# Optimization experiments

Hardware: AMD Instinct MI355X
Metric: run time of the kernel (lower is better)

The kernel has to match this reference:

```python
import jax, jax.numpy as jnp
import numpy as np

N, MA, F, NF = 512, 64, 128, 16
UPDATE_RATIO = 0.1
DECAY = 1.0
EPS = 1e-12  # avoids NaN grad of sqrt at self-distance 0 (torch diagonal is masked out by exp anyway)


def setup_inputs() -> dict:
    key = jax.random.key(0)
    ks = jax.random.split(key, 8)
    z = jax.random.randint(ks[0], (N, MA), 0, 10, dtype=jnp.int64) if jax.config.jax_enable_x64 else jax.random.randint(ks[0], (N, MA), 0, 10, dtype=jnp.int32)
    # pad last few atoms of each molecule with -1 to exercise the mask
    z = z.at[:, MA - 8:].set(-1)
    r = jax.random.normal(ks[1], (N, MA, 3), dtype=jnp.float32) * 3.0
    h = jax.random.normal(ks[2], (N, MA, F), dtype=jnp.float32)
    distances = jnp.linspace(0.5, 6.0, NF, dtype=jnp.float32)
    widths = jax.random.uniform(ks[3], (NF,), dtype=jnp.float32) * 0.5 + 0.5  # keep sigma > 0
    din = F * (1 + NF)  # 2176
    W1 = jax.random.normal(ks[4], (din, 512), dtype=jnp.float32) * (1.0 / np.sqrt(din))
    b1 = jnp.zeros((512,), dtype=jnp.float32)
    W2 = jax.random.normal(ks[5], (512, F), dtype=jnp.float32) * (1.0 / np.sqrt(512.0))
    b2 = jnp.zeros((F,), dtype=jnp.float32)
    return {"z": z, "r": r, "h": h, "distances": distances, "widths": widths,
            "W1": W1, "b1": b1, "W2": W2, "b2": b2}


def reference(z, r, h, distances, widths, W1, b1, W2, b2):
    n, ma = z.shape
    nf = distances.shape[0]
    # pairwise distance: (n, ma, ma)
    dv = r[:, :, None, :] - r[:, None, :, :]
    d = jnp.sqrt(jnp.sum(dv * dv, axis=-1) + EPS)
    mu = distances.reshape(1, nf, 1, 1)
    sigma = widths.reshape(1, nf, 1, 1)
    mask1 = (z > -1).astype(h.dtype)                      # (n, ma)
    pair_mask = mask1[:, :, None] * mask1[:, None, :]     # (n, ma, ma)
    # Gaussian RBF scores, masked: (n, nf, ma, ma)
    w = pair_mask[:, None] * jnp.exp(-((d[:, None] - mu) ** 2) / sigma) * 5.0
    # aggregate neighbor features: (n, ma, nf, F) -> (n, ma, nf*F)
    u = jnp.einsum('nfab,nbc->nafc', w, h).reshape(n, ma, nf * h.shape[-1])
    v = jnp.concatenate([h, u], axis=2)                   # (n, ma, F*(1+nf))
    v = jax.nn.silu(v @ W1 + b1) @ W2 + b2                # MLP 'net'
    h_new = h + v * UPDATE_RATIO * DECAY * mask1[:, :, None]
    return (z, r, h_new)
```

## Files before the change

kernel.cpp:

```cpp
#include <hip/hip_runtime.h>

#define MA 64
#define F 128
#define NF 16
#define HID 512
#define LDUB 144
#define WLB  9216
#define LDWB 144
#define LDT1B 1040

typedef float  float4v __attribute__((ext_vector_type(4)));
typedef short  short8  __attribute__((ext_vector_type(8)));
typedef int    int8v   __attribute__((ext_vector_type(8)));

static __device__ __forceinline__ unsigned int pack2bf(float x, float y) {
    unsigned int a = __float_as_uint(x) + 0x8000u;
    unsigned int b = __float_as_uint(y) + 0x8000u;
    return __builtin_amdgcn_perm(b, a, 0x07060302u);
}
static __device__ __forceinline__ unsigned short f2bf1(float x) {
    return (unsigned short)((__float_as_uint(x) + 0x8000u) >> 16);
}
static __device__ __forceinline__ unsigned int pk4fp8(float a, float b, float c, float d) {
    int p = __builtin_amdgcn_cvt_pk_fp8_f32(a, b, 0, false);
    p = __builtin_amdgcn_cvt_pk_fp8_f32(c, d, p, true);
    return (unsigned int)p;
}

__global__ void pack_frags(const float* __restrict__ W1, const float* __restrict__ W2,
                           unsigned char* __restrict__ w1p, unsigned short* __restrict__ w2p) {
    int gid  = blockIdx.x * 4 + (threadIdx.x >> 6);
    int lane = threadIdx.x & 63;
    int arow = lane & 15;
    int kq   = lane >> 4;
    if (gid < 544) {
        int kt = gid >> 5, jt = gid & 31;
        const float* base = W1 + (size_t)(kt * 128 + kq * 32) * HID + jt * 16 + arow;
        unsigned int o[8];
        #pragma unroll
        for (int p = 0; p < 8; p++)
            o[p] = pk4fp8(base[(p * 4 + 0) * HID], base[(p * 4 + 1) * HID],
                          base[(p * 4 + 2) * HID], base[(p * 4 + 3) * HID]);
        unsigned char* dst = w1p + ((size_t)gid * 64 + lane) * 32;
        *(uint4*)dst        = (uint4){o[0], o[1], o[2], o[3]};
        *(uint4*)(dst + 16) = (uint4){o[4], o[5], o[6], o[7]};
    } else if (gid < 544 + 128) {
        int g2 = gid - 544;
        int kt = g2 >> 3, mt = g2 & 7;
        const float* base = W2 + (size_t)(kt * 32 + kq * 8) * F + mt * 16 + arow;
        short8 o;
        #pragma unroll
        for (int j = 0; j < 8; j++) o[j] = (short)f2bf1(base[j * F]);
        *(short8*)(w2p + ((size_t)g2 * 64 + lane) * 8) = o;
    }
}

__launch_bounds__(512, 2)
__global__ void node_conv_mfma(const int* __restrict__ z, const float* __restrict__ rr,
        const float* __restrict__ h, const float* __restrict__ dist,
        const float* __restrict__ wid, const float* __restrict__ b1,
        const float* __restrict__ b2,
        const unsigned char* __restrict__ w1p, const unsigned short* __restrict__ w2p,
        float* __restrict__ out) {
    const int n = blockIdx.x;
    const int tid = threadIdx.x;
    const int lane = tid & 63;
    const int wave = tid >> 6;
    const int arow = lane & 15;
    const int quad = lane >> 4;
    const int kgrp = quad * 8;

    __shared__ __attribute__((aligned(16))) unsigned char lds[33280];
    __shared__ float r_lds[MA][4];

    const int N = gridDim.x;
    const float* hg = h + (size_t)n * MA * F;

    if (tid < MA) {
        int zi = z[n * MA + tid];
        out[(size_t)n * MA + tid] = (float)zi;
        r_lds[tid][0] = rr[(n * MA + tid) * 3 + 0];
        r_lds[tid][1] = rr[(n * MA + tid) * 3 + 1];
        r_lds[tid][2] = rr[(n * MA + tid) * 3 + 2];
        r_lds[tid][3] = (zi > -1) ? 1.0f : 0.0f;
    }
    if (tid < MA * 3)
        out[(size_t)N * MA + (size_t)n * MA * 3 + tid] = rr[(size_t)n * MA * 3 + tid];

    for (int i = tid; i < MA * F / 4; i += 512) {
        float4 v = ((const float4*)hg)[i];
        int a = i >> 5, c4 = (i & 31) * 4;
        *(unsigned int*)&lds[a * LDUB + c4] = pk4fp8(v.x, v.y, v.z, v.w);
    }
    short8 ah[2];
    {
        int c = wave * 16 + arow;
        #pragma unroll
        for (int ks2 = 0; ks2 < 2; ks2++)
            #pragma unroll
            for (int j = 0; j < 8; j++)
                ah[ks2][j] = (short)f2bf1(hg[(size_t)(ks2 * 32 + kgrp + j) * F + c]);
    }
    __syncthreads();

    const int wa = tid >> 3;
    const int wb0 = (tid & 7) * 8;
    float dpre[8];
    {
        float ax = r_lds[wa][0], ay = r_lds[wa][1], az = r_lds[wa][2];
        float am = r_lds[wa][3];
        #pragma unroll
        for (int j = 0; j < 8; j++) {
            float dx = ax - r_lds[wb0 + j][0];
            float dy = ay - r_lds[wb0 + j][1];
            float dz = az - r_lds[wb0 + j][2];
            float d = sqrtf(dx * dx + dy * dy + dz * dz + 1e-12f);
            float mm = am * r_lds[wb0 + j][3];
            dpre[j] = d + (1.0f - mm) * 1e4f;
        }
    }

    {
        float mu = dist[0];
        float isg = 1.0f / wid[0];
        float e[8];
        #pragma unroll
        for (int j = 0; j < 8; j++) {
            float t = dpre[j] - mu;
            e[j] = 5.0f * __expf(-t * t * isg);
        }
        uint4 wp = { pack2bf(e[0], e[1]), pack2bf(e[2], e[3]),
                     pack2bf(e[4], e[5]), pack2bf(e[6], e[7]) };
        *(uint4*)&lds[WLB + wa * LDWB + wb0 * 2] = wp;
    }
    int8v afr[4];
    #pragma unroll
    for (int mt = 0; mt < 4; mt++)
        afr[mt] = *(const int8v*)(w1p + ((size_t)((wave * 4 + mt) * 64 + lane)) * 32);
    __syncthreads();

    const float4v zf = {0.f, 0.f, 0.f, 0.f};
    float4v acc[4][4];
    #pragma unroll
    for (int i = 0; i < 4; i++)
        #pragma unroll
        for (int jv = 0; jv < 4; jv++) acc[i][jv] = zf;

    for (int f = 0; f <= NF; f++) {
        #pragma unroll
        for (int at = 0; at < 4; at++) {
            int8v bfr = *(const int8v*)&lds[(at * 16 + arow) * LDUB + quad * 32];
            #pragma unroll
            for (int mt = 0; mt < 4; mt++)
                acc[mt][at] = __builtin_amdgcn_mfma_scale_f32_16x16x128_f8f6f4(
                    afr[mt], bfr, acc[mt][at], 0, 0, 0, 127, 0, 127);
        }

        unsigned int udp[4];
        if (f < NF) {
            const unsigned char* pN = w1p + ((size_t)(((f + 1) * 32 + wave * 4) * 64 + lane)) * 32;
            #pragma unroll
            for (int mt = 0; mt < 4; mt++) afr[mt] = *(const int8v*)(pN + mt * 2048);

            float4v ud[4];
            #pragma unroll
            for (int at = 0; at < 4; at++) ud[at] = zf;
            #pragma unroll
            for (int ks2 = 0; ks2 < 2; ks2++)
                #pragma unroll
                for (int at = 0; at < 4; at++) {
                    short8 bw = *(const short8*)&lds[WLB + (at * 16 + arow) * LDWB + (ks2 * 32 + kgrp) * 2];
                    ud[at] = __builtin_amdgcn_mfma_f32_16x16x32_bf16(ah[ks2], bw, ud[at], 0, 0, 0);
                }
            #pragma unroll
            for (int at = 0; at < 4; at++)
                udp[at] = pk4fp8(ud[at][0], ud[at][1], ud[at][2], ud[at][3]);
        }
        __syncthreads();

        if (f < NF) {
            #pragma unroll
            for (int at = 0; at < 4; at++)
                *(unsigned int*)&lds[(at * 16 + arow) * LDUB + wave * 16 + quad * 4] = udp[at];

            if (f <= NF - 2) {
                float mu = dist[f + 1];
                float isg = 1.0f / wid[f + 1];
                float e[8];
                #pragma unroll
                for (int j = 0; j < 8; j++) {
                    float t = dpre[j] - mu;
                    e[j] = 5.0f * __expf(-t * t * isg);
                }
                uint4 wp = { pack2bf(e[0], e[1]), pack2bf(e[2], e[3]),
                             pack2bf(e[4], e[5]), pack2bf(e[6], e[7]) };
                *(uint4*)&lds[WLB + wa * LDWB + wb0 * 2] = wp;
            }
            __syncthreads();
        }
    }

    float4 b1v[4];
    #pragma unroll
    for (int mt = 0; mt < 4; mt++)
        b1v[mt] = *(const float4*)&b1[wave * 64 + mt * 16 + quad * 4];
    float* outh = out + (size_t)N * MA * 4 + (size_t)n * MA * F;

    #pragma unroll
    for (int hh = 0; hh < 2; hh++) {
        if (hh) __syncthreads();
        #pragma unroll
        for (int mt = 0; mt < 4; mt++) {
            #pragma unroll
            for (int ai = 0; ai < 2; ai++) {
                const int at = hh * 2 + ai;
                float xs[4];
                #pragma unroll
                for (int r = 0; r < 4; r++) {
                    float x = acc[mt][at][r] + ((const float*)&b1v[mt])[r];
                    xs[r] = x / (1.0f + __expf(-x));
                }
                uint2 pv = { pack2bf(xs[0], xs[1]), pack2bf(xs[2], xs[3]) };
                *(uint2*)&lds[(ai * 16 + arow) * LDT1B + (wave * 64 + mt * 16 + quad * 4) * 2] = pv;
            }
        }
        __syncthreads();

        float4v g2[2] = {zf, zf};
        for (int ks = 0; ks < 16; ks++) {
            short8 aw2 = *(const short8*)(w2p + ((size_t)(ks * 8 + wave) * 64 + lane) * 8);
            #pragma unroll
            for (int n2 = 0; n2 < 2; n2++) {
                short8 bt = *(const short8*)&lds[(n2 * 16 + arow) * LDT1B + (ks * 32 + kgrp) * 2];
                g2[n2] = __builtin_amdgcn_mfma_f32_16x16x32_bf16(aw2, bt, g2[n2], 0, 0, 0);
            }
        }
        #pragma unroll
        for (int n2 = 0; n2 < 2; n2++) {
            int a = hh * 32 + n2 * 16 + arow;
            int c0 = wave * 16 + quad * 4;
            float m = r_lds[a][3] * 0.1f;
            float4 hv = *(const float4*)&hg[a * F + c0];
            float4 b2v = *(const float4*)&b2[c0];
            float4 res;
            res.x = hv.x + (g2[n2][0] + b2v.x) * m;
            res.y = hv.y + (g2[n2][1] + b2v.y) * m;
            res.z = hv.z + (g2[n2][2] + b2v.z) * m;
            res.w = hv.w + (g2[n2][3] + b2v.w) * m;
            *(float4*)&outh[(size_t)a * F + c0] = res;
        }
    }
}

extern "C" void kernel_launch(void* const* d_in, const int* in_sizes, int n_in,
                              void* d_out, int out_size, void* d_ws, size_t ws_size,
                              hipStream_t stream) {
    const int*   z    = (const int*)d_in[0];
    const float* rr   = (const float*)d_in[1];
    const float* h    = (const float*)d_in[2];
    const float* dist = (const float*)d_in[3];
    const float* wid  = (const float*)d_in[4];
    const float* W1   = (const float*)d_in[5];
    const float* b1   = (const float*)d_in[6];
    const float* W2   = (const float*)d_in[7];
    const float* b2   = (const float*)d_in[8];
    float* out = (float*)d_out;

    int Nmol = in_sizes[0] / MA;

    unsigned char*  w1p = (unsigned char*)d_ws;
    unsigned short* w2p = (unsigned short*)(w1p + (size_t)544 * 64 * 32);

    pack_frags<<<168, 256, 0, stream>>>(W1, W2, w1p, w2p);
    node_conv_mfma<<<Nmol, 512, 0, stream>>>(z, rr, h, dist, wid, b1, b2, w1p, w2p, out);
}
```

Before: 152.8 us.

## Double-buffer LDS stages to drop per-iteration barrier and fuse second GEMM halves

Splits the fp8 u tile and bf16 RBF weight tile into ping-pong LDS buffers, so each filter iteration needs only one barrier instead of two. Replaces __syncthreads with an explicit lgkmcnt wait plus s_barrier. The second MLP layer now runs over all 64 atoms in one pass, with W2 fragments preloaded into registers. This doubles LDS use and raises register pressure, which could hurt occupancy or cause spills.

```diff
diff --git a/kernel.cpp b/kernel.cpp
--- a/kernel.cpp
+++ b/kernel.cpp
@@ -5,9 +5,12 @@
 #define NF 16
 #define HID 512
 #define LDUB 144
-#define WLB  9216
 #define LDWB 144
 #define LDT1B 1040
+#define UB0 0
+#define UB1 9216
+#define WL0 18432
+#define WL1 27648
 
 typedef float  float4v __attribute__((ext_vector_type(4)));
 typedef short  short8  __attribute__((ext_vector_type(8)));
@@ -26,6 +29,12 @@
     p = __builtin_amdgcn_cvt_pk_fp8_f32(c, d, p, true);
     return (unsigned int)p;
 }
+
+#define LGKM_BAR() do {                                        \
+    asm volatile("s_waitcnt lgkmcnt(0)" ::: "memory");         \
+    __builtin_amdgcn_s_barrier();                              \
+    asm volatile("" ::: "memory");                             \
+} while (0)
 
 __global__ void pack_frags(const float* __restrict__ W1, const float* __restrict__ W2,
                            unsigned char* __restrict__ w1p, unsigned short* __restrict__ w2p) {
@@ -70,8 +79,8 @@
     const int quad = lane >> 4;
     const int kgrp = quad * 8;
 
-    __shared__ __attribute__((aligned(16))) unsigned char lds[33280];
-    __shared__ float r_lds[MA][4];
+    __shared__ __attribute__((aligned(16))) unsigned char lds[66560];
+    __shared__ float r_lds[MA][5];
 
     const int N = gridDim.x;
     const float* hg = h + (size_t)n * MA * F;
@@ -90,7 +99,7 @@
     for (int i = tid; i < MA * F / 4; i += 512) {
         float4 v = ((const float4*)hg)[i];
         int a = i >> 5, c4 = (i & 31) * 4;
-        *(unsigned int*)&lds[a * LDUB + c4] = pk4fp8(v.x, v.y, v.z, v.w);
+        *(unsigned int*)&lds[UB0 + a * LDUB + c4] = pk4fp8(v.x, v.y, v.z, v.w);
     }
     short8 ah[2];
     {
@@ -131,13 +140,13 @@
         }
         uint4 wp = { pack2bf(e[0], e[1]), pack2bf(e[2], e[3]),
                      pack2bf(e[4], e[5]), pack2bf(e[6], e[7]) };
-        *(uint4*)&lds[WLB + wa * LDWB + wb0 * 2] = wp;
+        *(uint4*)&lds[WL0 + wa * LDWB + wb0 * 2] = wp;
     }
     int8v afr[4];
     #pragma unroll
     for (int mt = 0; mt < 4; mt++)
         afr[mt] = *(const int8v*)(w1p + ((size_t)((wave * 4 + mt) * 64 + lane)) * 32);
-    __syncthreads();
+    LGKM_BAR();
 
     const float4v zf = {0.f, 0.f, 0.f, 0.f};
     float4v acc[4][4];
@@ -147,16 +156,21 @@
         for (int jv = 0; jv < 4; jv++) acc[i][jv] = zf;
 
     for (int f = 0; f <= NF; f++) {
+        const int sel = f & 1;
+        const int ubR = sel ? UB1 : UB0;
+        const int ubW = sel ? UB0 : UB1;
+        const int wlR = sel ? WL1 : WL0;
+        const int wlW = sel ? WL0 : WL1;
+
         #pragma unroll
         for (int at = 0; at < 4; at++) {
-            int8v bfr = *(const int8v*)&lds[(at * 16 + arow) * LDUB + quad * 32];
+            int8v bfr = *(const int8v*)&lds[ubR + (at * 16 + arow) * LDUB + quad * 32];
             #pragma unroll
             for (int mt = 0; mt < 4; mt++)
                 acc[mt][at] = __builtin_amdgcn_mfma_scale_f32_16x16x128_f8f6f4(
                     afr[mt], bfr, acc[mt][at], 0, 0, 0, 127, 0, 127);
         }
 
-        unsigned int udp[4];
         if (f < NF) {
             const unsigned char* pN = w1p + ((size_t)(((f + 1) * 32 + wave * 4) * 64 + lane)) * 32;
             #pragma unroll
@@ -169,19 +183,14 @@
             for (int ks2 = 0; ks2 < 2; ks2++)
                 #pragma unroll
                 for (int at = 0; at < 4; at++) {
-                    short8 bw = *(const short8*)&lds[WLB + (at * 16 + arow) * LDWB + (ks2 * 32 + kgrp) * 2];
+                    short8 bw = *(const short8*)&lds[wlR + (at * 16 + arow) * LDWB + (ks2 * 32 + kgrp) * 2];
                     ud[at] = __builtin_amdgcn_mfma_f32_16x16x32_bf16(ah[ks2], bw, ud[at], 0, 0, 0);
                 }
             #pragma unroll
-            for (int at = 0; at < 4; at++)
-                udp[at] = pk4fp8(ud[at][0], ud[at][1], ud[at][2], ud[at][3]);
-        }
-        __syncthreads();
-
-        if (f < NF) {
-            #pragma unroll
-            for (int at = 0; at < 4; at++)
-                *(unsigned int*)&lds[(at * 16 + arow) * LDUB + wave * 16 + quad * 4] = udp[at];
+            for (int at = 0; at < 4; at++) {
+                unsigned int udp = pk4fp8(ud[at][0], ud[at][1], ud[at][2], ud[at][3]);
+                *(unsigned int*)&lds[ubW + (at * 16 + arow) * LDUB + wave * 16 + quad * 4] = udp;
+            }
 
             if (f <= NF - 2) {
                 float mu = dist[f + 1];
@@ -194,61 +203,65 @@
                 }
                 uint4 wp = { pack2bf(e[0], e[1]), pack2bf(e[2], e[3]),
                              pack2bf(e[4], e[5]), pack2bf(e[6], e[7]) };
-                *(uint4*)&lds[WLB + wa * LDWB + wb0 * 2] = wp;
+                *(uint4*)&lds[wlW + wa * LDWB + wb0 * 2] = wp;
             }
-            __syncthreads();
-        }
+        }
+        LGKM_BAR();
     }
 
     float4 b1v[4];
     #pragma unroll
     for (int mt = 0; mt < 4; mt++)
         b1v[mt] = *(const float4*)&b1[wave * 64 + mt * 16 + quad * 4];
+
+    short8 aw2r[16];
+    #pragma unroll
+    for (int ks = 0; ks < 16; ks++)
+        aw2r[ks] = *(const short8*)(w2p + ((size_t)(ks * 8 + wave) * 64 + lane) * 8);
+
+    #pragma unroll
+    for (int mt = 0; mt < 4; mt++) {
+        #pragma unroll
+        for (int at = 0; at < 4; at++) {
+            float xs[4];
+            #pragma unroll
+            for (int r = 0; r < 4; r++) {
+                float x = acc[mt][at][r] + ((const float*)&b1v[mt])[r];
+                xs[r] = x / (1.0f + __expf(-x));
+            }
+            uint2 pv = { pack2bf(xs[0], xs[1]), pack2bf(xs[2], xs[3]) };
+            *(uint2*)&lds[(at * 16 + arow) * LDT1B + (wave * 64 + mt * 16 + quad * 4) * 2] = pv;
+        }
+    }
+    LGKM_BAR();
+
+    float4v g2[4];
+    const float4v zf2 = {0.f, 0.f, 0.f, 0.f};
+    #pragma unroll
+    for (int n2 = 0; n2 < 4; n2++) g2[n2] = zf2;
+    #pragma unroll
+    for (int ks = 0; ks < 16; ks++) {
+        #pragma unroll
+        for (int n2 = 0; n2 < 4; n2++) {
+            short8 bt = *(const short8*)&lds[(n2 * 16 + arow) * LDT1B + (ks * 32 + kgrp) * 2];
+            g2[n2] = __builtin_amdgcn_mfma_f32_16x16x32_bf16(aw2r[ks], bt, g2[n2], 0, 0, 0);
+        }
+    }
+
     float* outh = out + (size_t)N * MA * 4 + (size_t)n * MA * F;
-
-    #pragma unroll
-    for (int hh = 0; hh < 2; hh++) {
-        if (hh) __syncthreads();
-        #pragma unroll
-        for (int mt = 0; mt < 4; mt++) {
-            #pragma unroll
-            for (int ai = 0; ai < 2; ai++) {
-                const int at = hh * 2 + ai;
-                float xs[4];
-                #pragma unroll
-                for (int r = 0; r < 4; r++) {
-                    float x = acc[mt][at][r] + ((const float*)&b1v[mt])[r];
-                    xs[r] = x / (1.0f + __expf(-x));
-                }
-                uint2 pv = { pack2bf(xs[0], xs[1]), pack2bf(xs[2], xs[3]) };
-                *(uint2*)&lds[(ai * 16 + arow) * LDT1B + (wave * 64 + mt * 16 + quad * 4) * 2] = pv;
-            }
-        }
-        __syncthreads();
-
-        float4v g2[2] = {zf, zf};
-        for (int ks = 0; ks < 16; ks++) {
-            short8 aw2 = *(const short8*)(w2p + ((size_t)(ks * 8 + wave) * 64 + lane) * 8);
-            #pragma unroll
-            for (int n2 = 0; n2 < 2; n2++) {
-                short8 bt = *(const short8*)&lds[(n2 * 16 + arow) * LDT1B + (ks * 32 + kgrp) * 2];
-                g2[n2] = __builtin_amdgcn_mfma_f32_16x16x32_bf16(aw2, bt, g2[n2], 0, 0, 0);
-            }
-        }
-        #pragma unroll
-        for (int n2 = 0; n2 < 2; n2++) {
-            int a = hh * 32 + n2 * 16 + arow;
-            int c0 = wave * 16 + quad * 4;
-            float m = r_lds[a][3] * 0.1f;
-            float4 hv = *(const float4*)&hg[a * F + c0];
-            float4 b2v = *(const float4*)&b2[c0];
-            float4 res;
-            res.x = hv.x + (g2[n2][0] + b2v.x) * m;
-            res.y = hv.y + (g2[n2][1] + b2v.y) * m;
-            res.z = hv.z + (g2[n2][2] + b2v.z) * m;
-            res.w = hv.w + (g2[n2][3] + b2v.w) * m;
-            *(float4*)&outh[(size_t)a * F + c0] = res;
-        }
+    const int c0 = wave * 16 + quad * 4;
+    float4 b2v = *(const float4*)&b2[c0];
+    #pragma unroll
+    for (int n2 = 0; n2 < 4; n2++) {
+        int a = n2 * 16 + arow;
+        float m = r_lds[a][3] * 0.1f;
+        float4 hv = *(const float4*)&hg[a * F + c0];
+        float4 res;
+        res.x = hv.x + (g2[n2][0] + b2v.x) * m;
+        res.y = hv.y + (g2[n2][1] + b2v.y) * m;
+        res.z = hv.z + (g2[n2][2] + b2v.z) * m;
+        res.w = hv.w + (g2[n2][3] + b2v.w) * m;
+        *(float4*)&outh[(size_t)a * F + c0] = res;
     }
 }
 
```

Result: faster. 145.7 us (-4.7%).
